# Kernel tuning notes

Measured on AMD Instinct MI355X. Metric: run time of the kernel, lower is better.

Reference implementation:

```python
import jax, jax.numpy as jnp
import numpy as np

EPS = 1e-3


def batchnorm(x, gamma, beta):
    # BatchNorm1d in training mode: batch mean and biased variance over dim 0
    mean = jnp.mean(x, axis=0)
    var = jnp.var(x, axis=0)  # biased, matches torch BN normalization
    return (x - mean) * jax.lax.rsqrt(var + EPS) * gamma + beta


def setup_inputs() -> dict:
    key = jax.random.key(0)
    ks = jax.random.split(key, 12)
    N, C_in, C_out, G = 400000, 64, 128, 30000
    points_xyz = jax.random.normal(ks[0], (N, 3), dtype=jnp.float32) * 10.0
    feat_all = jax.random.normal(ks[1], (N, C_in), dtype=jnp.float32)
    unq_inv = jax.random.randint(ks[2], (N,), 0, G, dtype=jnp.int32)
    s_in = 1.0 / np.sqrt(C_in)
    s3 = 1.0 / np.sqrt(3.0)
    return {
        "points_xyz": points_xyz,
        "feat_all": feat_all,
        "unq_inv": unq_inv,
        "W_pre": jax.random.uniform(ks[3], (C_in, C_out), jnp.float32, -s_in, s_in),
        "b_pre": jax.random.uniform(ks[4], (C_out,), jnp.float32, -s_in, s_in),
        "g1": jnp.ones((C_out,), jnp.float32),
        "be1": jnp.zeros((C_out,), jnp.float32),
        "Wp1": jax.random.uniform(ks[5], (3, C_out), jnp.float32, -s3, s3),
        "bp1": jax.random.uniform(ks[6], (C_out,), jnp.float32, -s3, s3),
        "Wp2": jax.random.uniform(ks[7], (3, C_out), jnp.float32, -s3, s3),
        "bp2": jax.random.uniform(ks[8], (C_out,), jnp.float32, -s3, s3),
        "g2": jnp.ones((C_out,), jnp.float32),
        "be2": jnp.zeros((C_out,), jnp.float32),
        "num_segments": 30000,
    }


def reference(points_xyz, feat_all, unq_inv, W_pre, b_pre, g1, be1,
              Wp1, bp1, Wp2, bp2, g2, be2, num_segments):
    p = jnp.floor(points_xyz)                       # [N, 3]
    feat = batchnorm(feat_all @ W_pre + b_pre, g1, be1)  # [N, C_out]
    pw1 = p @ Wp1 + bp1                             # [N, C_out]
    pw2 = p @ Wp2 + bp2                             # [N, C_out]
    feat_weight = pw1 * feat                        # [N, C_out]
    feat_add = jax.ops.segment_sum(feat_weight, unq_inv,
                                   num_segments=num_segments)  # [G, C_out]
    feat_add = feat_add[unq_inv]                    # gather back: [N, C_out]
    out = pw2 * feat - feat_add
    out = jax.nn.relu(batchnorm(out, g2, be2))
    return out
```

## Files before the change

### kernel.cpp

```cpp
#include <hip/hip_runtime.h>
#include <hip/hip_bf16.h>

typedef unsigned int u32;
typedef unsigned short u16;
typedef __attribute__((ext_vector_type(8))) short short8;
typedef __attribute__((ext_vector_type(4))) float floatx4;

#define COUT 128
#define GSEG 30000
#define BN_EPS 1e-3f
#define REP 32

__device__ __forceinline__ u32 f2bf(float x) {
    u32 u = __float_as_uint(x);
    return (u + 0x7fffu + ((u >> 16) & 1u)) >> 16;
}
__device__ __forceinline__ float bf2f(u32 b) { return __uint_as_float(b << 16); }

__device__ __forceinline__ void unpack8(uint4 v, float* f) {
    f[0] = __uint_as_float(v.x << 16); f[1] = __uint_as_float(v.x & 0xffff0000u);
    f[2] = __uint_as_float(v.y << 16); f[3] = __uint_as_float(v.y & 0xffff0000u);
    f[4] = __uint_as_float(v.z << 16); f[5] = __uint_as_float(v.z & 0xffff0000u);
    f[6] = __uint_as_float(v.w << 16); f[7] = __uint_as_float(v.w & 0xffff0000u);
}

__global__ __launch_bounds__(512) void k_prep_w(
    const float* __restrict__ W, u16* __restrict__ wt_f)
{
    int t = threadIdx.x;
    for (int f = t; f < 8192; f += 512) {
        int ch = f >> 3, e = f & 7;
        int ct = ch >> 7, ks = (ch >> 6) & 1, lane = ch & 63;
        int c = ct * 16 + (lane & 15);
        int k = ks * 32 + (lane >> 4) * 8 + e;
        float w = W[k * 128 + c];
        u32 hb = f2bf(w);
        float lo = w - bf2f(hb);
        wt_f[f] = (u16)hb;
        wt_f[8192 + f] = (u16)f2bf(lo);
    }
}

__global__ __launch_bounds__(512) void k_gemm_bn1(
    const float* __restrict__ A, const u16* __restrict__ wt_f,
    const float* __restrict__ bias, const int* __restrict__ unq, int* __restrict__ cnt,
    u16* __restrict__ lin, float* __restrict__ sum1rep, float* __restrict__ sumsq1rep, int n)
{
    __shared__ union {
        u16 w[16384];
        u16 pack[128 * 136];
    } sm;
    __shared__ float sSum[128], sSq[128];

    const int t = threadIdx.x;
    const int row0 = blockIdx.x * 128;
    if (t < 128) { sSum[t] = 0.f; sSq[t] = 0.f; }

    if (t < 128 && row0 + t < n) atomicAdd(&cnt[unq[row0 + t]], 1);

    const int lane = t & 63, wv = t >> 6;
    const int r = lane & 15, q = lane >> 4;
    const int rw0 = wv * 16;
    const int row_a = row0 + rw0 + r;
    const bool ok = row_a < n;

    const float* ap = A + (size_t)row_a * 64;
    float4 av[4];
#pragma unroll
    for (int ks = 0; ks < 2; ks++) {
        av[ks * 2]     = ok ? *(const float4*)(ap + ks * 32 + q * 8)     : make_float4(0.f, 0.f, 0.f, 0.f);
        av[ks * 2 + 1] = ok ? *(const float4*)(ap + ks * 32 + q * 8 + 4) : make_float4(0.f, 0.f, 0.f, 0.f);
    }

#pragma unroll
    for (int j = 0; j < 4; j++) {
        int chunk = j * 512 + t;
        uint4 v = *(const uint4*)(wt_f + chunk * 8);
        *(uint4*)&sm.w[chunk * 8] = v;
    }

    short8 arh[2], arl[2];
#pragma unroll
    for (int ks = 0; ks < 2; ks++) {
        float vv[8] = {av[ks * 2].x, av[ks * 2].y, av[ks * 2].z, av[ks * 2].w,
                       av[ks * 2 + 1].x, av[ks * 2 + 1].y, av[ks * 2 + 1].z, av[ks * 2 + 1].w};
#pragma unroll
        for (int i = 0; i < 8; i++) {
            u32 hb = f2bf(vv[i]);
            float lo = vv[i] - bf2f(hb);
            arh[ks][i] = (short)(u16)hb;
            arl[ks][i] = (short)(u16)f2bf(lo);
        }
    }

    floatx4 acc[8];
#pragma unroll
    for (int ct = 0; ct < 8; ct++) acc[ct] = (floatx4){0.f, 0.f, 0.f, 0.f};

    __syncthreads();

    const int fbase = lane * 8;
#pragma unroll
    for (int ct = 0; ct < 8; ct++) {
#pragma unroll
        for (int ks = 0; ks < 2; ks++) {
            int fo = (ct * 2 + ks) * 512 + fbase;
            short8 wh = *(const short8*)&sm.w[fo];
            short8 wl = *(const short8*)&sm.w[8192 + fo];
            acc[ct] = __builtin_amdgcn_mfma_f32_16x16x32_bf16(arh[ks], wh, acc[ct], 0, 0, 0);
            acc[ct] = __builtin_amdgcn_mfma_f32_16x16x32_bf16(arl[ks], wh, acc[ct], 0, 0, 0);
            acc[ct] = __builtin_amdgcn_mfma_f32_16x16x32_bf16(arh[ks], wl, acc[ct], 0, 0, 0);
        }
    }
    __syncthreads();

#pragma unroll
    for (int ct = 0; ct < 8; ct++) {
        int c = ct * 16 + r;
        float bv = bias[c];
        float ssum = 0.f, ssq = 0.f;
#pragma unroll
        for (int i = 0; i < 4; i++) {
            int lrow = rw0 + q * 4 + i;
            float v = acc[ct][i] + bv;
            if (row0 + lrow >= n) v = 0.f;
            ssum += v; ssq += v * v;
            sm.pack[lrow * 136 + c] = (u16)f2bf(v);
        }
        ssum += __shfl_xor(ssum, 16, 64); ssq += __shfl_xor(ssq, 16, 64);
        ssum += __shfl_xor(ssum, 32, 64); ssq += __shfl_xor(ssq, 32, 64);
        if (lane < 16) { atomicAdd(&sSum[c], ssum); atomicAdd(&sSq[c], ssq); }
    }
    __syncthreads();

#pragma unroll
    for (int j = 0; j < 4; j++) {
        int f = t + j * 512;
        int row = f >> 4, c0 = (f & 15) << 3;
        if (row0 + row < n) {
            uint4 v = *(const uint4*)&sm.pack[row * 136 + c0];
            *(uint4*)(lin + (size_t)(row0 + row) * 128 + c0) = v;
        }
    }
    if (t < 128) {
        int rep = (blockIdx.x & (REP - 1)) * 128;
        atomicAdd(&sum1rep[rep + t], sSum[t]);
        atomicAdd(&sumsq1rep[rep + t], sSq[t]);
    }
}

__global__ void k_fin(const float* __restrict__ sumrep, const float* __restrict__ sqrep,
                      const float* __restrict__ g, const float* __restrict__ be,
                      float* __restrict__ scale, float* __restrict__ shift, float inv_n)
{
    int c = threadIdx.x;
    float s = 0.f, q = 0.f;
#pragma unroll
    for (int r = 0; r < REP; r++) { s += sumrep[r * 128 + c]; q += sqrep[r * 128 + c]; }
    float mean = s * inv_n;
    float var = q * inv_n - mean * mean;
    float sc = g[c] * rsqrtf(var + BN_EPS);
    scale[c] = sc;
    shift[c] = be[c] - mean * sc;
}

__global__ __launch_bounds__(1024) void k_scan(const int* __restrict__ cnt,
                                               int* __restrict__ offs,
                                               int* __restrict__ cursor)
{
    __shared__ int wsum[16];
    int t = threadIdx.x, lane = t & 63, wv = t >> 6;
    int base = t * 32;
    int v[32];
    int s = 0;
    if (base + 32 <= GSEG) {
        const int4* cp = (const int4*)(cnt + base);
#pragma unroll
        for (int j = 0; j < 8; j++) {
            int4 q = cp[j];
            v[j * 4 + 0] = q.x; v[j * 4 + 1] = q.y; v[j * 4 + 2] = q.z; v[j * 4 + 3] = q.w;
            s += q.x + q.y + q.z + q.w;
        }
    } else {
#pragma unroll
        for (int j = 0; j < 32; j++) {
            int idx = base + j;
            int x = (idx < GSEG) ? cnt[idx] : 0;
            v[j] = x; s += x;
        }
    }
    int x = s;
#pragma unroll
    for (int d = 1; d < 64; d <<= 1) {
        int u = __shfl_up(x, d, 64);
        if (lane >= d) x += u;
    }
    if (lane == 63) wsum[wv] = x;
    __syncthreads();
    if (t < 16) {
        int w = wsum[t];
#pragma unroll
        for (int d = 1; d < 16; d <<= 1) {
            int u = __shfl_up(w, d, 16);
            if (t >= d) w += u;
        }
        wsum[t] = w;
    }
    __syncthreads();
    int run = (wv ? wsum[wv - 1] : 0) + (x - s);
#pragma unroll
    for (int j = 0; j < 32; j++) {
        int idx = base + j;
        if (idx < GSEG) { offs[idx] = run; cursor[idx] = run; }
        run += v[j];
    }
    if (t == 1023) offs[GSEG] = wsum[15];
}

__global__ __launch_bounds__(256) void k_scatter_idx(const int* __restrict__ unq,
                                                     int* __restrict__ cursor,
                                                     int* __restrict__ order, int n)
{
    int i = blockIdx.x * 256 + threadIdx.x;
    if (i < n) {
        int pos = atomicAdd(&cursor[unq[i]], 1);
        order[pos] = i;
    }
}

__global__ __launch_bounds__(256) void k_segsum(
    const u16* __restrict__ lin, const float* __restrict__ xyz,
    const int* __restrict__ order, const int* __restrict__ offs,
    const float* __restrict__ scale1, const float* __restrict__ shift1,
    const float* __restrict__ Wp1, const float* __restrict__ bp1,
    const float* __restrict__ Wp2, const float* __restrict__ bp2,
    float* __restrict__ feat_add, float* __restrict__ sum2rep, float* __restrict__ sumsq2rep,
    int nseg)
{
    __shared__ float sSum[128], sSq[128];
    const int t = threadIdx.x;
    if (t < 128) { sSum[t] = 0.f; sSq[t] = 0.f; }
    __syncthreads();
    const int wave = t >> 6, lane = t & 63;
    const int c = lane * 2;
    const float wa0x = Wp1[c],     wa0y = Wp1[128 + c],     wa0z = Wp1[256 + c],     ba0 = bp1[c];
    const float wa1x = Wp1[c + 1], wa1y = Wp1[128 + c + 1], wa1z = Wp1[256 + c + 1], ba1 = bp1[c + 1];
    const float wb0x = Wp2[c],     wb0y = Wp2[128 + c],     wb0z = Wp2[256 + c],     bb0 = bp2[c];
    const float wb1x = Wp2[c + 1], wb1y = Wp2[128 + c + 1], wb1z = Wp2[256 + c + 1], bb1 = bp2[c + 1];
    const float sc0 = scale1[c], sh0 = shift1[c];
    const float sc1 = scale1[c + 1], sh1 = shift1[c + 1];
    float rs0 = 0.f, rs1 = 0.f, rq0 = 0.f, rq1 = 0.f;
    const int stride = gridDim.x * 4;
    for (int s = blockIdx.x * 4 + wave; s < nseg; s += stride) {
        const int beg = offs[s], end = offs[s + 1];
        const int m = end - beg;
        int rowv = 0; float fxv = 0.f, fyv = 0.f, fzv = 0.f;
        if (lane < m) {
            rowv = order[beg + lane];
            float2 xy = *(const float2*)(xyz + rowv * 3);
            fxv = floorf(xy.x);
            fyv = floorf(xy.y);
            fzv = floorf(xyz[rowv * 3 + 2]);
        }
        float acc0 = 0.f, acc1 = 0.f, p10 = 0.f, p11 = 0.f, p20 = 0.f, p21 = 0.f;
        const int mm = m < 64 ? m : 64;
        int j = 0;
        for (; j + 2 <= mm; j += 2) {
            int rowA = __shfl(rowv, j, 64),     rowB = __shfl(rowv, j + 1, 64);
            float pxA = __shfl(fxv, j, 64),     pxB = __shfl(fxv, j + 1, 64);
            float pyA = __shfl(fyv, j, 64),     pyB = __shfl(fyv, j + 1, 64);
            float pzA = __shfl(fzv, j, 64),     pzB = __shfl(fzv, j + 1, 64);
            u32 lA = *(const u32*)(lin + (size_t)rowA * 128 + c);
            u32 lB = *(const u32*)(lin + (size_t)rowB * 128 + c);
            float feA0 = fmaf(__uint_as_float(lA << 16), sc0, sh0);
            float feA1 = fmaf(__uint_as_float(lA & 0xffff0000u), sc1, sh1);
            float feB0 = fmaf(__uint_as_float(lB << 16), sc0, sh0);
            float feB1 = fmaf(__uint_as_float(lB & 0xffff0000u), sc1, sh1);
            float paA0 = fmaf(pxA, wa0x, fmaf(pyA, wa0y, fmaf(pzA, wa0z, ba0)));
            float paA1 = fmaf(pxA, wa1x, fmaf(pyA, wa1y, fmaf(pzA, wa1z, ba1)));
            float pbA0 = fmaf(pxA, wb0x, fmaf(pyA, wb0y, fmaf(pzA, wb0z, bb0)));
            float pbA1 = fmaf(pxA, wb1x, fmaf(pyA, wb1y, fmaf(pzA, wb1z, bb1)));
            float paB0 = fmaf(pxB, wa0x, fmaf(pyB, wa0y, fmaf(pzB, wa0z, ba0)));
            float paB1 = fmaf(pxB, wa1x, fmaf(pyB, wa1y, fmaf(pzB, wa1z, ba1)));
            float pbB0 = fmaf(pxB, wb0x, fmaf(pyB, wb0y, fmaf(pzB, wb0z, bb0)));
            float pbB1 = fmaf(pxB, wb1x, fmaf(pyB, wb1y, fmaf(pzB, wb1z, bb1)));
            acc0 = fmaf(paA0, feA0, acc0); acc1 = fmaf(paA1, feA1, acc1);
            float tA0 = pbA0 * feA0, tA1 = pbA1 * feA1;
            p10 += tA0; p11 += tA1;
            p20 = fmaf(tA0, tA0, p20); p21 = fmaf(tA1, tA1, p21);
            acc0 = fmaf(paB0, feB0, acc0); acc1 = fmaf(paB1, feB1, acc1);
            float tB0 = pbB0 * feB0, tB1 = pbB1 * feB1;
            p10 += tB0; p11 += tB1;
            p20 = fmaf(tB0, tB0, p20); p21 = fmaf(tB1, tB1, p21);
        }
        for (; j < mm; j++) {
            int row = __shfl(rowv, j, 64);
            float px = __shfl(fxv, j, 64);
            float py = __shfl(fyv, j, 64);
            float pz = __shfl(fzv, j, 64);
            u32 l2 = *(const u32*)(lin + (size_t)row * 128 + c);
            float fe0 = fmaf(__uint_as_float(l2 << 16), sc0, sh0);
            float fe1 = fmaf(__uint_as_float(l2 & 0xffff0000u), sc1, sh1);
            float pa0 = fmaf(px, wa0x, fmaf(py, wa0y, fmaf(pz, wa0z, ba0)));
            float pa1 = fmaf(px, wa1x, fmaf(py, wa1y, fmaf(pz, wa1z, ba1)));
            float pb0 = fmaf(px, wb0x, fmaf(py, wb0y, fmaf(pz, wb0z, bb0)));
            float pb1 = fmaf(px, wb1x, fmaf(py, wb1y, fmaf(pz, wb1z, bb1)));
            acc0 = fmaf(pa0, fe0, acc0);
            acc1 = fmaf(pa1, fe1, acc1);
            float t0 = pb0 * fe0, t1 = pb1 * fe1;
            p10 += t0; p11 += t1;
            p20 = fmaf(t0, t0, p20); p21 = fmaf(t1, t1, p21);
        }
        for (int jj = 64; jj < m; jj++) {
            int row = order[beg + jj];
            float px = floorf(xyz[row * 3]);
            float py = floorf(xyz[row * 3 + 1]);
            float pz = floorf(xyz[row * 3 + 2]);
            u32 l2 = *(const u32*)(lin + (size_t)row * 128 + c);
            float fe0 = fmaf(__uint_as_float(l2 << 16), sc0, sh0);
            float fe1 = fmaf(__uint_as_float(l2 & 0xffff0000u), sc1, sh1);
            float pa0 = fmaf(px, wa0x, fmaf(py, wa0y, fmaf(pz, wa0z, ba0)));
            float pa1 = fmaf(px, wa1x, fmaf(py, wa1y, fmaf(pz, wa1z, ba1)));
            float pb0 = fmaf(px, wb0x, fmaf(py, wb0y, fmaf(pz, wb0z, bb0)));
            float pb1 = fmaf(px, wb1x, fmaf(py, wb1y, fmaf(pz, wb1z, bb1)));
            acc0 = fmaf(pa0, fe0, acc0);
            acc1 = fmaf(pa1, fe1, acc1);
            float t0 = pb0 * fe0, t1 = pb1 * fe1;
            p10 += t0; p11 += t1;
            p20 = fmaf(t0, t0, p20); p21 = fmaf(t1, t1, p21);
        }
        float2 st; st.x = acc0; st.y = acc1;
        *(float2*)(feat_add + (size_t)s * 128 + c) = st;
        float fm = (float)m;
        rs0 += p10 - fm * acc0;
        rs1 += p11 - fm * acc1;
        rq0 += fmaf(fm * acc0, acc0, p20 - 2.f * acc0 * p10);
        rq1 += fmaf(fm * acc1, acc1, p21 - 2.f * acc1 * p11);
    }
    atomicAdd(&sSum[c], rs0); atomicAdd(&sSum[c + 1], rs1);
    atomicAdd(&sSq[c], rq0);  atomicAdd(&sSq[c + 1], rq1);
    __syncthreads();
    if (t < 128) {
        int rep = (blockIdx.x & (REP - 1)) * 128;
        atomicAdd(&sum2rep[rep + t], sSum[t]);
        atomicAdd(&sumsq2rep[rep + t], sSq[t]);
    }
}

__global__ __launch_bounds__(256) void k_final(
    const u16* __restrict__ lin, const float* __restrict__ xyz, const int* __restrict__ unq,
    const float* __restrict__ scale1, const float* __restrict__ shift1,
    const float* __restrict__ Wp2, const float* __restrict__ bp2,
    const float* __restrict__ feat_add,
    const float* __restrict__ scale2, const float* __restrict__ shift2,
    float* __restrict__ out, int n)
{
    __shared__ float sS[128], sH[128], sW3[384], sB[128], sS2[128], sH2[128];
    int t = threadIdx.x;
    if (t < 128) {
        sS[t] = scale1[t]; sH[t] = shift1[t]; sB[t] = bp2[t];
        sW3[t] = Wp2[t]; sW3[128 + t] = Wp2[128 + t]; sW3[256 + t] = Wp2[256 + t];
        sS2[t] = scale2[t]; sH2[t] = shift2[t];
    }
    __syncthreads();
    int row = blockIdx.x * 16 + (t >> 4);
    if (row >= n) return;
    int c0 = (t & 15) * 8;
    uint4 l8 = *(const uint4*)(lin + (size_t)row * 128 + c0);
    float f[8];
    unpack8(l8, f);
    float px = floorf(xyz[row * 3 + 0]);
    float py = floorf(xyz[row * 3 + 1]);
    float pz = floorf(xyz[row * 3 + 2]);
    int g = unq[row];
    const float4* fa = (const float4*)(feat_add + (size_t)g * 128 + c0);
    float4 fa0 = fa[0], fa1 = fa[1];
    float fav[8] = {fa0.x, fa0.y, fa0.z, fa0.w, fa1.x, fa1.y, fa1.z, fa1.w};
    float o[8];
#pragma unroll
    for (int j = 0; j < 8; j++) {
        int c = c0 + j;
        float fe = fmaf(f[j], sS[c], sH[c]);
        float pw = fmaf(px, sW3[c], fmaf(py, sW3[128 + c], fmaf(pz, sW3[256 + c], sB[c])));
        float v = pw * fe - fav[j];
        v = fmaf(v, sS2[c], sH2[c]);
        o[j] = v > 0.f ? v : 0.f;
    }
    float4 s0, s1;
    s0.x = o[0]; s0.y = o[1]; s0.z = o[2]; s0.w = o[3];
    s1.x = o[4]; s1.y = o[5]; s1.z = o[6]; s1.w = o[7];
    float* op = out + (size_t)row * 128 + c0;
    *(float4*)op = s0;
    *(float4*)(op + 4) = s1;
}

extern "C" void kernel_launch(void* const* d_in, const int* in_sizes, int n_in,
                              void* d_out, int out_size, void* d_ws, size_t ws_size,
                              hipStream_t stream)
{
    const float* xyz      = (const float*)d_in[0];
    const float* feat_all = (const float*)d_in[1];
    const int*   unq      = (const int*)d_in[2];
    const float* W_pre    = (const float*)d_in[3];
    const float* b_pre    = (const float*)d_in[4];
    const float* g1       = (const float*)d_in[5];
    const float* be1      = (const float*)d_in[6];
    const float* Wp1      = (const float*)d_in[7];
    const float* bp1      = (const float*)d_in[8];
    const float* Wp2      = (const float*)d_in[9];
    const float* bp2      = (const float*)d_in[10];
    const float* g2       = (const float*)d_in[11];
    const float* be2      = (const float*)d_in[12];
    (void)n_in; (void)out_size; (void)ws_size;

    const int n = in_sizes[0] / 3;

    char* ws = (char*)d_ws;
    float* sum1rep   = (float*)(ws + 0);
    float* sumsq1rep = (float*)(ws + 16384);
    float* sum2rep   = (float*)(ws + 32768);
    float* sumsq2rep = (float*)(ws + 49152);
    float* scale1    = (float*)(ws + 65536);
    float* shift1    = (float*)(ws + 66048);
    float* scale2    = (float*)(ws + 66560);
    float* shift2    = (float*)(ws + 67072);
    int*   offs      = (int*)(ws + 67584);
    int*   cursor    = (int*)(ws + 187648);
    u16*   wt_f      = (u16*)(ws + 187648);
    int*   order     = (int*)(ws + 307648);
    int*   cnt       = (int*)(ws + 307648);
    float* feat_add  = (float*)(ws + 1907648);
    u16*   lin       = (u16*)(ws + 17267648);

    hipMemsetAsync(ws, 0, 65536, stream);
    hipMemsetAsync(ws + 307648, 0, 120000, stream);

    k_prep_w<<<1, 512, 0, stream>>>(W_pre, wt_f);
    k_gemm_bn1<<<(n + 127) / 128, 512, 0, stream>>>(feat_all, wt_f, b_pre, unq, cnt,
                                                    lin, sum1rep, sumsq1rep, n);
    k_fin<<<1, 128, 0, stream>>>(sum1rep, sumsq1rep, g1, be1, scale1, shift1, 1.0f / n);

    k_scan<<<1, 1024, 0, stream>>>(cnt, offs, cursor);
    k_scatter_idx<<<(n + 255) / 256, 256, 0, stream>>>(unq, cursor, order, n);
    k_segsum<<<1876, 256, 0, stream>>>(lin, xyz, order, offs, scale1, shift1,
                                       Wp1, bp1, Wp2, bp2, feat_add, sum2rep, sumsq2rep, GSEG);
    k_fin<<<1, 128, 0, stream>>>(sum2rep, sumsq2rep, g2, be2, scale2, shift2, 1.0f / n);
    k_final<<<(n + 15) / 16, 256, 0, stream>>>(lin, xyz, unq, scale1, shift1, Wp2, bp2,
                                               feat_add, scale2, shift2, (float*)d_out, n);
}
```

Before: 529.8 us.

## Process four row tiles per GEMM block with register prefetch; unroll segsum by four

The GEMM+BN1 kernel now handles 512 rows per block in four 128-row iterations. It loads the weight tile into shared memory once per block and double-buffers the next tile's A rows in registers while the current tile runs through MFMA. BN statistics are kept in registers across iterations, and outputs are written straight to global memory instead of being staged through shared memory, which removes two block barriers. The trade-off is narrow 2-byte scattered stores that are less coalesced. The segment-sum inner loop is unrolled from two rows to four so more gather loads are in flight at once, at the cost of higher register use.

```diff
diff --git a/kernel.cpp b/kernel.cpp
--- a/kernel.cpp
+++ b/kernel.cpp
@@ -46,102 +46,115 @@
     const float* __restrict__ bias, const int* __restrict__ unq, int* __restrict__ cnt,
     u16* __restrict__ lin, float* __restrict__ sum1rep, float* __restrict__ sumsq1rep, int n)
 {
-    __shared__ union {
-        u16 w[16384];
-        u16 pack[128 * 136];
-    } sm;
+    __shared__ u16 smw[16384];
     __shared__ float sSum[128], sSq[128];
 
     const int t = threadIdx.x;
-    const int row0 = blockIdx.x * 128;
+    const int base = blockIdx.x * 512;
     if (t < 128) { sSum[t] = 0.f; sSq[t] = 0.f; }
 
-    if (t < 128 && row0 + t < n) atomicAdd(&cnt[unq[row0 + t]], 1);
+    if (base + t < n) atomicAdd(&cnt[unq[base + t]], 1);
 
     const int lane = t & 63, wv = t >> 6;
     const int r = lane & 15, q = lane >> 4;
     const int rw0 = wv * 16;
-    const int row_a = row0 + rw0 + r;
-    const bool ok = row_a < n;
-
-    const float* ap = A + (size_t)row_a * 64;
-    float4 av[4];
-#pragma unroll
-    for (int ks = 0; ks < 2; ks++) {
-        av[ks * 2]     = ok ? *(const float4*)(ap + ks * 32 + q * 8)     : make_float4(0.f, 0.f, 0.f, 0.f);
-        av[ks * 2 + 1] = ok ? *(const float4*)(ap + ks * 32 + q * 8 + 4) : make_float4(0.f, 0.f, 0.f, 0.f);
-    }
 
 #pragma unroll
     for (int j = 0; j < 4; j++) {
         int chunk = j * 512 + t;
-        uint4 v = *(const uint4*)(wt_f + chunk * 8);
-        *(uint4*)&sm.w[chunk * 8] = v;
-    }
-
-    short8 arh[2], arl[2];
-#pragma unroll
-    for (int ks = 0; ks < 2; ks++) {
-        float vv[8] = {av[ks * 2].x, av[ks * 2].y, av[ks * 2].z, av[ks * 2].w,
-                       av[ks * 2 + 1].x, av[ks * 2 + 1].y, av[ks * 2 + 1].z, av[ks * 2 + 1].w};
-#pragma unroll
-        for (int i = 0; i < 8; i++) {
-            u32 hb = f2bf(vv[i]);
-            float lo = vv[i] - bf2f(hb);
-            arh[ks][i] = (short)(u16)hb;
-            arl[ks][i] = (short)(u16)f2bf(lo);
-        }
-    }
-
-    floatx4 acc[8];
-#pragma unroll
-    for (int ct = 0; ct < 8; ct++) acc[ct] = (floatx4){0.f, 0.f, 0.f, 0.f};
-
-    __syncthreads();
+        *(uint4*)&smw[chunk * 8] = *(const uint4*)(wt_f + chunk * 8);
+    }
+
+    float4 av[2][4];
+    {
+        int row_a = base + rw0 + r;
+        const float* ap = A + (size_t)row_a * 64;
+        bool ok = row_a < n;
+#pragma unroll
+        for (int ks = 0; ks < 2; ks++) {
+            av[0][ks * 2]     = ok ? *(const float4*)(ap + ks * 32 + q * 8)     : make_float4(0.f, 0.f, 0.f, 0.f);
+            av[0][ks * 2 + 1] = ok ? *(const float4*)(ap + ks * 32 + q * 8 + 4) : make_float4(0.f, 0.f, 0.f, 0.f);
+        }
+    }
+    __syncthreads();
+
+    float bv[8];
+#pragma unroll
+    for (int ct = 0; ct < 8; ct++) bv[ct] = bias[ct * 16 + r];
+
+    float ssum[8], ssq[8];
+#pragma unroll
+    for (int ct = 0; ct < 8; ct++) { ssum[ct] = 0.f; ssq[ct] = 0.f; }
 
     const int fbase = lane * 8;
+
+#pragma unroll
+    for (int it = 0; it < 4; it++) {
+        const int cur = it & 1, nxt = cur ^ 1;
+        if (it < 3) {
+            int row_n = base + (it + 1) * 128 + rw0 + r;
+            const float* ap = A + (size_t)row_n * 64;
+            bool ok = row_n < n;
+#pragma unroll
+            for (int ks = 0; ks < 2; ks++) {
+                av[nxt][ks * 2]     = ok ? *(const float4*)(ap + ks * 32 + q * 8)     : make_float4(0.f, 0.f, 0.f, 0.f);
+                av[nxt][ks * 2 + 1] = ok ? *(const float4*)(ap + ks * 32 + q * 8 + 4) : make_float4(0.f, 0.f, 0.f, 0.f);
+            }
+        }
+        short8 arh[2], arl[2];
+#pragma unroll
+        for (int ks = 0; ks < 2; ks++) {
+            float vv[8] = {av[cur][ks * 2].x, av[cur][ks * 2].y, av[cur][ks * 2].z, av[cur][ks * 2].w,
+                           av[cur][ks * 2 + 1].x, av[cur][ks * 2 + 1].y, av[cur][ks * 2 + 1].z, av[cur][ks * 2 + 1].w};
+#pragma unroll
+            for (int i = 0; i < 8; i++) {
+                u32 hb = f2bf(vv[i]);
+                float lo = vv[i] - bf2f(hb);
+                arh[ks][i] = (short)(u16)hb;
+                arl[ks][i] = (short)(u16)f2bf(lo);
+            }
+        }
+
+        floatx4 acc[8];
+#pragma unroll
+        for (int ct = 0; ct < 8; ct++) acc[ct] = (floatx4){0.f, 0.f, 0.f, 0.f};
+
+#pragma unroll
+        for (int ct = 0; ct < 8; ct++) {
+#pragma unroll
+            for (int ks = 0; ks < 2; ks++) {
+                int fo = (ct * 2 + ks) * 512 + fbase;
+                short8 wh = *(const short8*)&smw[fo];
+                short8 wl = *(const short8*)&smw[8192 + fo];
+                acc[ct] = __builtin_amdgcn_mfma_f32_16x16x32_bf16(arh[ks], wh, acc[ct], 0, 0, 0);
+                acc[ct] = __builtin_amdgcn_mfma_f32_16x16x32_bf16(arl[ks], wh, acc[ct], 0, 0, 0);
+                acc[ct] = __builtin_amdgcn_mfma_f32_16x16x32_bf16(arh[ks], wl, acc[ct], 0, 0, 0);
+            }
+        }
+
+#pragma unroll
+        for (int ct = 0; ct < 8; ct++) {
+            int c = ct * 16 + r;
+#pragma unroll
+            for (int i = 0; i < 4; i++) {
+                int grow = base + it * 128 + rw0 + q * 4 + i;
+                float v = acc[ct][i] + bv[ct];
+                if (grow < n) {
+                    ssum[ct] += v; ssq[ct] += v * v;
+                    lin[(size_t)grow * 128 + c] = (u16)f2bf(v);
+                }
+            }
+        }
+    }
+
 #pragma unroll
     for (int ct = 0; ct < 8; ct++) {
-#pragma unroll
-        for (int ks = 0; ks < 2; ks++) {
-            int fo = (ct * 2 + ks) * 512 + fbase;
-            short8 wh = *(const short8*)&sm.w[fo];
-            short8 wl = *(const short8*)&sm.w[8192 + fo];
-            acc[ct] = __builtin_amdgcn_mfma_f32_16x16x32_bf16(arh[ks], wh, acc[ct], 0, 0, 0);
-            acc[ct] = __builtin_amdgcn_mfma_f32_16x16x32_bf16(arl[ks], wh, acc[ct], 0, 0, 0);
-            acc[ct] = __builtin_amdgcn_mfma_f32_16x16x32_bf16(arh[ks], wl, acc[ct], 0, 0, 0);
-        }
-    }
-    __syncthreads();
-
-#pragma unroll
-    for (int ct = 0; ct < 8; ct++) {
-        int c = ct * 16 + r;
-        float bv = bias[c];
-        float ssum = 0.f, ssq = 0.f;
-#pragma unroll
-        for (int i = 0; i < 4; i++) {
-            int lrow = rw0 + q * 4 + i;
-            float v = acc[ct][i] + bv;
-            if (row0 + lrow >= n) v = 0.f;
-            ssum += v; ssq += v * v;
-            sm.pack[lrow * 136 + c] = (u16)f2bf(v);
-        }
-        ssum += __shfl_xor(ssum, 16, 64); ssq += __shfl_xor(ssq, 16, 64);
-        ssum += __shfl_xor(ssum, 32, 64); ssq += __shfl_xor(ssq, 32, 64);
-        if (lane < 16) { atomicAdd(&sSum[c], ssum); atomicAdd(&sSq[c], ssq); }
-    }
-    __syncthreads();
-
-#pragma unroll
-    for (int j = 0; j < 4; j++) {
-        int f = t + j * 512;
-        int row = f >> 4, c0 = (f & 15) << 3;
-        if (row0 + row < n) {
-            uint4 v = *(const uint4*)&sm.pack[row * 136 + c0];
-            *(uint4*)(lin + (size_t)(row0 + row) * 128 + c0) = v;
-        }
-    }
+        float s = ssum[ct], qq = ssq[ct];
+        s += __shfl_xor(s, 16, 64); qq += __shfl_xor(qq, 16, 64);
+        s += __shfl_xor(s, 32, 64); qq += __shfl_xor(qq, 32, 64);
+        if (lane < 16) { atomicAdd(&sSum[ct * 16 + r], s); atomicAdd(&sSq[ct * 16 + r], qq); }
+    }
+    __syncthreads();
     if (t < 128) {
         int rep = (blockIdx.x & (REP - 1)) * 128;
         atomicAdd(&sum1rep[rep + t], sSum[t]);
@@ -265,33 +278,32 @@
         float acc0 = 0.f, acc1 = 0.f, p10 = 0.f, p11 = 0.f, p20 = 0.f, p21 = 0.f;
         const int mm = m < 64 ? m : 64;
         int j = 0;
-        for (; j + 2 <= mm; j += 2) {
-            int rowA = __shfl(rowv, j, 64),     rowB = __shfl(rowv, j + 1, 64);
-            float pxA = __shfl(fxv, j, 64),     pxB = __shfl(fxv, j + 1, 64);
-            float pyA = __shfl(fyv, j, 64),     pyB = __shfl(fyv, j + 1, 64);
-            float pzA = __shfl(fzv, j, 64),     pzB = __shfl(fzv, j + 1, 64);
-            u32 lA = *(const u32*)(lin + (size_t)rowA * 128 + c);
-            u32 lB = *(const u32*)(lin + (size_t)rowB * 128 + c);
-            float feA0 = fmaf(__uint_as_float(lA << 16), sc0, sh0);
-            float feA1 = fmaf(__uint_as_float(lA & 0xffff0000u), sc1, sh1);
-            float feB0 = fmaf(__uint_as_float(lB << 16), sc0, sh0);
-            float feB1 = fmaf(__uint_as_float(lB & 0xffff0000u), sc1, sh1);
-            float paA0 = fmaf(pxA, wa0x, fmaf(pyA, wa0y, fmaf(pzA, wa0z, ba0)));
-            float paA1 = fmaf(pxA, wa1x, fmaf(pyA, wa1y, fmaf(pzA, wa1z, ba1)));
-            float pbA0 = fmaf(pxA, wb0x, fmaf(pyA, wb0y, fmaf(pzA, wb0z, bb0)));
-            float pbA1 = fmaf(pxA, wb1x, fmaf(pyA, wb1y, fmaf(pzA, wb1z, bb1)));
-            float paB0 = fmaf(pxB, wa0x, fmaf(pyB, wa0y, fmaf(pzB, wa0z, ba0)));
-            float paB1 = fmaf(pxB, wa1x, fmaf(pyB, wa1y, fmaf(pzB, wa1z, ba1)));
-            float pbB0 = fmaf(pxB, wb0x, fmaf(pyB, wb0y, fmaf(pzB, wb0z, bb0)));
-            float pbB1 = fmaf(pxB, wb1x, fmaf(pyB, wb1y, fmaf(pzB, wb1z, bb1)));
-            acc0 = fmaf(paA0, feA0, acc0); acc1 = fmaf(paA1, feA1, acc1);
-            float tA0 = pbA0 * feA0, tA1 = pbA1 * feA1;
-            p10 += tA0; p11 += tA1;
-            p20 = fmaf(tA0, tA0, p20); p21 = fmaf(tA1, tA1, p21);
-            acc0 = fmaf(paB0, feB0, acc0); acc1 = fmaf(paB1, feB1, acc1);
-            float tB0 = pbB0 * feB0, tB1 = pbB1 * feB1;
-            p10 += tB0; p11 += tB1;
-            p20 = fmaf(tB0, tB0, p20); p21 = fmaf(tB1, tB1, p21);
+        for (; j + 4 <= mm; j += 4) {
+            int   rw[4]; float px[4], py[4], pz[4]; u32 ll[4];
+#pragma unroll
+            for (int k = 0; k < 4; k++) {
+                rw[k] = __shfl(rowv, j + k, 64);
+                px[k] = __shfl(fxv, j + k, 64);
+                py[k] = __shfl(fyv, j + k, 64);
+                pz[k] = __shfl(fzv, j + k, 64);
+            }
+#pragma unroll
+            for (int k = 0; k < 4; k++)
+                ll[k] = *(const u32*)(lin + (size_t)rw[k] * 128 + c);
+#pragma unroll
+            for (int k = 0; k < 4; k++) {
+                float fe0 = fmaf(__uint_as_float(ll[k] << 16), sc0, sh0);
+                float fe1 = fmaf(__uint_as_float(ll[k] & 0xffff0000u), sc1, sh1);
+                float pa0 = fmaf(px[k], wa0x, fmaf(py[k], wa0y, fmaf(pz[k], wa0z, ba0)));
+                float pa1 = fmaf(px[k], wa1x, fmaf(py[k], wa1y, fmaf(pz[k], wa1z, ba1)));
+                float pb0 = fmaf(px[k], wb0x, fmaf(py[k], wb0y, fmaf(pz[k], wb0z, bb0)));
+                float pb1 = fmaf(px[k], wb1x, fmaf(py[k], wb1y, fmaf(pz[k], wb1z, bb1)));
+                acc0 = fmaf(pa0, fe0, acc0);
+                acc1 = fmaf(pa1, fe1, acc1);
+                float t0 = pb0 * fe0, t1 = pb1 * fe1;
+                p10 += t0; p11 += t1;
+                p20 = fmaf(t0, t0, p20); p21 = fmaf(t1, t1, p21);
+            }
         }
         for (; j < mm; j++) {
             int row = __shfl(rowv, j, 64);
@@ -436,7 +448,7 @@
     hipMemsetAsync(ws + 307648, 0, 120000, stream);
 
     k_prep_w<<<1, 512, 0, stream>>>(W_pre, wt_f);
-    k_gemm_bn1<<<(n + 127) / 128, 512, 0, stream>>>(feat_all, wt_f, b_pre, unq, cnt,
+    k_gemm_bn1<<<(n + 511) / 512, 512, 0, stream>>>(feat_all, wt_f, b_pre, unq, cnt,
                                                     lin, sum1rep, sumsq1rep, n);
     k_fin<<<1, 128, 0, stream>>>(sum1rep, sumsq1rep, g1, be1, scale1, shift1, 1.0f / n);
 
```

New measurement: 519.3 us. 1.02x faster.
